# Performance work log

Hardware: AMD Instinct MI355X
Metric: run time of the kernel (lower is better)

Reference implementation:

```python
import jax, jax.numpy as jnp
import numpy as np

EMBED_DIM = 2048
NUM_HEADS = 32
NUM_KV_HEADS = 8
HEAD_DIM = EMBED_DIM // NUM_HEADS  # 64
KV_DIM = HEAD_DIM * NUM_KV_HEADS   # 512
ROPE_BASE = 10000.0


def rope_cos_sin(seq_len, dim):
    inv_freq = 1.0 / (ROPE_BASE ** (jnp.arange(0, dim, 2, dtype=jnp.float32) / dim))
    t = jnp.arange(seq_len, dtype=jnp.float32)
    freqs = jnp.outer(t, inv_freq)                 # [T, dim/2]
    emb = jnp.concatenate([freqs, freqs], axis=-1)  # [T, dim]
    return jnp.cos(emb), jnp.sin(emb)


def rotate_half(x):
    half = x.shape[-1] // 2
    return jnp.concatenate([-x[..., half:], x[..., :half]], axis=-1)


def setup_inputs() -> dict:
    key = jax.random.key(0)
    k_x, k_q, k_k, k_v, k_o = jax.random.split(key, 5)
    B, T, C = 2, 2048, EMBED_DIM
    s = 1.0 / np.sqrt(C)
    x = jax.random.normal(k_x, (B, T, C), dtype=jnp.float32)
    # Linear weights stored as [in, out]; no bias (bias=False)
    Wq = jax.random.normal(k_q, (C, EMBED_DIM), dtype=jnp.float32) * s
    Wk = jax.random.normal(k_k, (C, KV_DIM), dtype=jnp.float32) * s
    Wv = jax.random.normal(k_v, (C, KV_DIM), dtype=jnp.float32) * s
    Wo = jax.random.normal(k_o, (C, EMBED_DIM), dtype=jnp.float32) * s
    return {"x": x, "Wq": Wq, "Wk": Wk, "Wv": Wv, "Wo": Wo}


def reference(x, Wq, Wk, Wv, Wo):
    B, T, C = x.shape
    H, KVH, D = NUM_HEADS, NUM_KV_HEADS, HEAD_DIM
    scale = D ** -0.5
    rep = H // KVH

    q = (x @ Wq).reshape(B, T, H, D).transpose(0, 2, 1, 3)    # [B,H,T,D]
    k = (x @ Wk).reshape(B, T, KVH, D).transpose(0, 2, 1, 3)  # [B,KVH,T,D]
    v = (x @ Wv).reshape(B, T, KVH, D).transpose(0, 2, 1, 3)
    # repeat_interleave over head dim to expand KV heads
    k = jnp.repeat(k, rep, axis=1)  # [B,H,T,D]
    v = jnp.repeat(v, rep, axis=1)

    cos, sin = rope_cos_sin(T, D)
    cos = cos[None, None, :, :]
    sin = sin[None, None, :, :]
    q = q * cos + rotate_half(q) * sin
    k = k * cos + rotate_half(k) * sin

    att = jnp.einsum('bhtd,bhsd->bhts', q, k) * scale  # [B,H,T,T]
    att = jax.nn.softmax(att, axis=-1)                 # mask=None, dropout eval
    y = jnp.einsum('bhts,bhsd->bhtd', att, v)          # [B,H,T,D]
    y = y.transpose(0, 2, 1, 3).reshape(B, T, C)
    return y @ Wo
```

## Files before the change

kernel.cpp:

```cpp
#include <hip/hip_runtime.h>
#include <stdint.h>

#define Tn   2048
#define Cn   2048
#define Hn   32
#define KVHn 8
#define Dn   64
#define MR   4096
#define NQKV 3072
#define KD   2048

typedef __attribute__((ext_vector_type(4))) float fx4;
typedef __attribute__((ext_vector_type(8))) short frag8;

#define MFMA(a,b,c) __builtin_amdgcn_mfma_f32_16x16x32_bf16((a),(b),(c),0,0,0)

struct __align__(16) U16x8 { unsigned short s[8]; };

__device__ __forceinline__ unsigned short f2bf(float x){
  union { float f; unsigned u; } v; v.f = x;
  return (unsigned short)((v.u + 0x7FFFu + ((v.u >> 16) & 1u)) >> 16);
}
__device__ __forceinline__ float bf2f(unsigned short h){
  union { unsigned u; float f; } v; v.u = ((unsigned)h) << 16; return v.f;
}
__device__ __forceinline__ float sexp2(float x){
#if __has_builtin(__builtin_amdgcn_exp2f)
  return __builtin_amdgcn_exp2f(x);
#else
  return exp2f(x);
#endif
}
__device__ __forceinline__ unsigned cvtpk(float a, float b){
  unsigned r; asm("v_cvt_pk_bf16_f32 %0, %1, %2" : "=v"(r) : "v"(a), "v"(b)); return r;
}

typedef const __attribute__((address_space(1))) void cas1_void;
typedef __attribute__((address_space(3))) void as3_void;
__device__ __forceinline__ void gld16(const void* g, void* l){
  __builtin_amdgcn_global_load_lds((cas1_void*)g, (as3_void*)l, 16, 0, 0);
}

__global__ __launch_bounds__(256) void k_cvt(const float* __restrict__ in,
                                             unsigned short* __restrict__ out){
  size_t i = (size_t)blockIdx.x * 256 + threadIdx.x;
  float4 v = *(const float4*)(in + i * 4);
  ushort4 o; o.x = f2bf(v.x); o.y = f2bf(v.y); o.z = f2bf(v.z); o.w = f2bf(v.w);
  *(ushort4*)(out + i * 4) = o;
}

__global__ __launch_bounds__(256) void k_transW(const float* __restrict__ W0,
                                                const float* __restrict__ W1,
                                                const float* __restrict__ W2,
                                                unsigned short* __restrict__ out){
  __shared__ float tile[64][65];
  int n0 = blockIdx.x * 64, k0 = blockIdx.y * 64;
  const float* src; int col0, ld;
  if (n0 < 2048)      { src = W0; col0 = n0;        ld = 2048; }
  else if (n0 < 2560) { src = W1; col0 = n0 - 2048; ld = 512;  }
  else                { src = W2; col0 = n0 - 2560; ld = 512;  }
  int t = threadIdx.x;
  int r = t >> 2, cc = (t & 3) << 4;
  const float* p = src + (size_t)(k0 + r) * ld + col0 + cc;
  #pragma unroll
  for (int j = 0; j < 16; j += 4) {
    float4 v = *(const float4*)(p + j);
    tile[r][cc + j + 0] = v.x; tile[r][cc + j + 1] = v.y;
    tile[r][cc + j + 2] = v.z; tile[r][cc + j + 3] = v.w;
  }
  __syncthreads();
  int n = t >> 2, kc = (t & 3) << 4;
  unsigned short* q = out + (size_t)(n0 + n) * 2048 + k0 + kc;
  U16x8 o0, o1;
  #pragma unroll
  for (int j = 0; j < 8; ++j) o0.s[j] = f2bf(tile[kc + j][n]);
  #pragma unroll
  for (int j = 0; j < 8; ++j) o1.s[j] = f2bf(tile[kc + 8 + j][n]);
  *(U16x8*)(q) = o0;
  *(U16x8*)(q + 8) = o1;
}

__global__ __launch_bounds__(256) void k_ropetab(float* __restrict__ ct, float* __restrict__ st){
  int i = blockIdx.x * 256 + threadIdx.x;
  int tp = i >> 5, d = i & 31;
  float inv = powf(10000.0f, -(float)d * (1.0f/32.0f));
  float fr = (float)tp * inv;
  ct[i] = cosf(fr); st[i] = sinf(fr);
}

template<int OUT_BF16>
__global__ __launch_bounds__(256) void k_gemm(const unsigned short* __restrict__ A,
                                              const unsigned short* __restrict__ Bt,
                                              void* __restrict__ Cp,
                                              int M, int N, int K){
  __shared__ unsigned short As[128 * 64];
  __shared__ unsigned short Bs[128 * 64];
  int tid = threadIdx.x;
  int m0 = blockIdx.y * 128, n0 = blockIdx.x * 128;
  int w = tid >> 6, ln = tid & 63, lr = ln & 15, lg = ln >> 4;
  int wm = (w >> 1) * 64, wn = (w & 1) * 64;
  fx4 acc[4][4];
  #pragma unroll
  for (int i = 0; i < 4; ++i)
    #pragma unroll
    for (int j = 0; j < 4; ++j) acc[i][j] = (fx4){0.f,0.f,0.f,0.f};
  int steps = K >> 6;
  for (int kt = 0; kt < steps; ++kt) {
    int kb = kt << 6;
    #pragma unroll
    for (int it = 0; it < 4; ++it) {
      int nch = it * 256 + tid;
      int r = nch >> 3, c = (nch & 7) ^ (r & 7);
      gld16(A  + (size_t)(m0 + r) * K + kb + c * 8, (char*)As + nch * 16);
      gld16(Bt + (size_t)(n0 + r) * K + kb + c * 8, (char*)Bs + nch * 16);
    }
    __syncthreads();
    frag8 aF[4][2], bF[4][2];
    #pragma unroll
    for (int i = 0; i < 4; ++i) {
      int ra = wm + i * 16 + lr;
      int rb = wn + i * 16 + lr;
      #pragma unroll
      for (int kk = 0; kk < 2; ++kk) {
        aF[i][kk] = *(const frag8*)((const char*)As + ra * 128 + (((lg + 4*kk) ^ (ra & 7)) << 4));
        bF[i][kk] = *(const frag8*)((const char*)Bs + rb * 128 + (((lg + 4*kk) ^ (rb & 7)) << 4));
      }
    }
    #pragma unroll
    for (int kk = 0; kk < 2; ++kk)
      #pragma unroll
      for (int i = 0; i < 4; ++i)
        #pragma unroll
        for (int j = 0; j < 4; ++j)
          acc[i][j] = MFMA(aF[i][kk], bF[j][kk], acc[i][j]);
    __syncthreads();
  }
  #pragma unroll
  for (int i = 0; i < 4; ++i) {
    int row = m0 + wm + i * 16 + lg * 4;
    #pragma unroll
    for (int j = 0; j < 4; ++j) {
      int col = n0 + wn + j * 16 + lr;
      #pragma unroll
      for (int rr = 0; rr < 4; ++rr) {
        if (OUT_BF16) ((unsigned short*)Cp)[(size_t)(row + rr) * N + col] = f2bf(acc[i][j][rr]);
        else          ((float*)Cp)[(size_t)(row + rr) * N + col] = acc[i][j][rr];
      }
    }
  }
}

__global__ __launch_bounds__(256) void k_rope(unsigned short* __restrict__ qkv,
                                              const float* __restrict__ ct,
                                              const float* __restrict__ st){
  int idx = blockIdx.x * 256 + threadIdx.x;
  int p4 = idx & 7;
  int rest = idx >> 3;
  int hh = rest % 40;
  int row = rest / 40;
  int tpos = row & (Tn - 1);
  int colbase = (hh < 32) ? (hh << 6) : (2048 + ((hh - 32) << 6));
  int d0 = p4 << 2;
  unsigned short* base = qkv + (size_t)row * NQKV + colbase + d0;
  ushort4 av = *(const ushort4*)(base);
  ushort4 bv = *(const ushort4*)(base + 32);
  float4 c4 = *(const float4*)(ct + (tpos << 5) + d0);
  float4 s4 = *(const float4*)(st + (tpos << 5) + d0);
  float sc = (hh < 32) ? 0.180336880f : 1.0f;
  float a0 = bf2f(av.x), a1 = bf2f(av.y), a2 = bf2f(av.z), a3 = bf2f(av.w);
  float b0 = bf2f(bv.x), b1 = bf2f(bv.y), b2 = bf2f(bv.z), b3 = bf2f(bv.w);
  ushort4 ra, rb;
  ra.x = f2bf((a0 * c4.x - b0 * s4.x) * sc);
  ra.y = f2bf((a1 * c4.y - b1 * s4.y) * sc);
  ra.z = f2bf((a2 * c4.z - b2 * s4.z) * sc);
  ra.w = f2bf((a3 * c4.w - b3 * s4.w) * sc);
  rb.x = f2bf((b0 * c4.x + a0 * s4.x) * sc);
  rb.y = f2bf((b1 * c4.y + a1 * s4.y) * sc);
  rb.z = f2bf((b2 * c4.z + a2 * s4.z) * sc);
  rb.w = f2bf((b3 * c4.w + a3 * s4.w) * sc);
  *(ushort4*)(base)      = ra;
  *(ushort4*)(base + 32) = rb;
}

__global__ __launch_bounds__(256) void k_vt(const unsigned short* __restrict__ qkv,
                                            unsigned short* __restrict__ vt){
  __shared__ unsigned short tl[64][66];
  int head = blockIdx.y;
  int b = head >> 3, kvh = head & 7;
  int t0 = blockIdx.x * 64;
  int t = threadIdx.x;
  int r = t >> 2, cc = (t & 3) << 4;
  const unsigned short* p = qkv + (size_t)(b * Tn + t0 + r) * NQKV + 2560 + kvh * 64 + cc;
  U16x8 v0 = *(const U16x8*)(p);
  U16x8 v1 = *(const U16x8*)(p + 8);
  #pragma unroll
  for (int j = 0; j < 8; ++j) { tl[r][cc + j] = v0.s[j]; tl[r][cc + 8 + j] = v1.s[j]; }
  __syncthreads();
  int d = t >> 2, cpair = t & 3;
  unsigned short* q = vt + ((size_t)head * 64 + d) * Tn + t0;
  #pragma unroll
  for (int ci = 0; ci < 2; ++ci) {
    int c = cpair * 2 + ci;
    U16x8 oo;
    #pragma unroll
    for (int e = 0; e < 8; ++e)
      oo.s[e] = tl[32 * (c >> 2) + 16 * (e >> 2) + 4 * (c & 3) + (e & 3)][d];
    *(U16x8*)(q + c * 8) = oo;
  }
}

__global__ __launch_bounds__(256) void k_attn(const unsigned short* __restrict__ qkv,
                                              const unsigned short* __restrict__ vt,
                                              unsigned short* __restrict__ y){
  __shared__ unsigned short Ks[2][64 * 64];
  __shared__ unsigned short Vs[2][64 * 64];
  int tid = threadIdx.x, w = tid >> 6, ln = tid & 63, lq = ln & 15, lg = ln >> 4;
  int bh = blockIdx.y, b = bh >> 5, h = bh & 31, kvh = h >> 2;
  int q0 = blockIdx.x * 128;
  frag8 qF[2][2];
  #pragma unroll
  for (int s = 0; s < 2; ++s) {
    const unsigned short* qrow = qkv + (size_t)(b * Tn + q0 + w * 32 + 16 * s + lq) * NQKV + h * 64;
    qF[s][0] = *(const frag8*)(qrow + lg * 8);
    qF[s][1] = *(const frag8*)(qrow + 32 + lg * 8);
  }
  int n0 = tid, n1 = 256 + tid;
  int r0 = n0 >> 3, c0 = (n0 & 7) ^ (r0 & 7);
  int r1 = n1 >> 3, c1 = (n1 & 7) ^ (r1 & 7);
  const unsigned short* kp0 = qkv + (size_t)b * Tn * NQKV + 2048 + kvh * 64 + (size_t)r0 * NQKV + c0 * 8;
  const unsigned short* kp1 = qkv + (size_t)b * Tn * NQKV + 2048 + kvh * 64 + (size_t)r1 * NQKV + c1 * 8;
  const unsigned short* vp0 = vt + ((size_t)(b * 8 + kvh) * 64 + r0) * Tn + c0 * 8;
  const unsigned short* vp1 = vt + ((size_t)(b * 8 + kvh) * 64 + r1) * Tn + c1 * 8;
  int koff0 = lq * 128 + (((lg)     ^ (lq & 7)) << 4);
  int koff1 = lq * 128 + (((lg + 4) ^ (lq & 7)) << 4);

#define STAGE(BUF) do {                                      \
    gld16(kp0, (char*)&Ks[BUF][0] + n0 * 16);                \
    gld16(kp1, (char*)&Ks[BUF][0] + n1 * 16);                \
    gld16(vp0, (char*)&Vs[BUF][0] + n0 * 16);                \
    gld16(vp1, (char*)&Vs[BUF][0] + n1 * 16);                \
    kp0 += 64 * NQKV; kp1 += 64 * NQKV; vp0 += 64; vp1 += 64;\
  } while (0)

#define PB(S, KK) ({ union { unsigned u[4]; frag8 f; } t_;                        \
    t_.u[0] = pu[S][2*(KK)][0]; t_.u[1] = pu[S][2*(KK)][1];                       \
    t_.u[2] = pu[S][2*(KK)+1][0]; t_.u[3] = pu[S][2*(KK)+1][1]; t_.f; })

#define COMPUTE(BUF) do {                                                         \
    const char* kb_ = (const char*)&Ks[BUF][0];                                   \
    const char* vb_ = (const char*)&Vs[BUF][0];                                   \
    frag8 kf[4][2];                                                               \
    _Pragma("unroll")                                                             \
    for (int mf = 0; mf < 4; ++mf) {                                              \
      kf[mf][0] = *(const frag8*)(kb_ + mf * 2048 + koff0);                       \
      kf[mf][1] = *(const frag8*)(kb_ + mf * 2048 + koff1);                       \
    }                                                                             \
    fx4 sf[2][4];                                                                 \
    __builtin_amdgcn_s_setprio(1);                                                \
    _Pragma("unroll")                                                             \
    for (int s = 0; s < 2; ++s)                                                   \
      _Pragma("unroll")                                                           \
      for (int mf = 0; mf < 4; ++mf) {                                            \
        sf[s][mf] = (fx4){0.f, 0.f, 0.f, 0.f};                                    \
        sf[s][mf] = MFMA(kf[mf][0], qF[s][0], sf[s][mf]);                         \
        sf[s][mf] = MFMA(kf[mf][1], qF[s][1], sf[s][mf]);                         \
      }                                                                           \
    __builtin_amdgcn_s_setprio(0);                                                \
    unsigned pu[2][4][2];                                                         \
    _Pragma("unroll")                                                             \
    for (int s = 0; s < 2; ++s) {                                                 \
      float ps = 0.f;                                                             \
      _Pragma("unroll")                                                           \
      for (int mf = 0; mf < 4; ++mf) {                                            \
        float p0 = sexp2(sf[s][mf][0]);                                           \
        float p1 = sexp2(sf[s][mf][1]);                                           \
        float p2 = sexp2(sf[s][mf][2]);                                           \
        float p3 = sexp2(sf[s][mf][3]);                                           \
        ps += (p0 + p1) + (p2 + p3);                                              \
        pu[s][mf][0] = cvtpk(p0, p1);                                             \
        pu[s][mf][1] = cvtpk(p2, p3);                                             \
      }                                                                           \
      lpart[s] += ps;                                                             \
    }                                                                             \
    frag8 vf[4][2];                                                               \
    _Pragma("unroll")                                                             \
    for (int df = 0; df < 4; ++df) {                                              \
      vf[df][0] = *(const frag8*)(vb_ + df * 2048 + koff0);                       \
      vf[df][1] = *(const frag8*)(vb_ + df * 2048 + koff1);                       \
    }                                                                             \
    __builtin_amdgcn_s_setprio(1);                                                \
    _Pragma("unroll")                                                             \
    for (int s = 0; s < 2; ++s)                                                   \
      _Pragma("unroll")                                                           \
      for (int df = 0; df < 4; ++df) {                                            \
        o[s][df] = MFMA(vf[df][0], PB(s, 0), o[s][df]);                           \
        o[s][df] = MFMA(vf[df][1], PB(s, 1), o[s][df]);                           \
      }                                                                           \
    __builtin_amdgcn_s_setprio(0);                                                \
  } while (0)

  fx4 o[2][4];
  float lpart[2] = {0.f, 0.f};
  #pragma unroll
  for (int s = 0; s < 2; ++s)
    #pragma unroll
    for (int i = 0; i < 4; ++i) o[s][i] = (fx4){0.f, 0.f, 0.f, 0.f};

  STAGE(0);
  __syncthreads();
  for (int kt = 0; kt < 32; kt += 2) {
    STAGE(1);
    COMPUTE(0);
    __syncthreads();
    if (kt + 2 < 32) STAGE(0);
    COMPUTE(1);
    __syncthreads();
  }
#undef STAGE
#undef COMPUTE
#undef PB

  #pragma unroll
  for (int s = 0; s < 2; ++s) {
    lpart[s] += __shfl_xor(lpart[s], 16);
    lpart[s] += __shfl_xor(lpart[s], 32);
    float inv = 1.0f / lpart[s];
    unsigned short* yp = y + (size_t)(b * Tn + q0 + w * 32 + 16 * s + lq) * Cn + h * 64;
    #pragma unroll
    for (int df = 0; df < 4; ++df) {
      unsigned lo = cvtpk(o[s][df][0] * inv, o[s][df][1] * inv);
      unsigned hi = cvtpk(o[s][df][2] * inv, o[s][df][3] * inv);
      *(uint2*)(yp + df * 16 + lg * 4) = make_uint2(lo, hi);
    }
  }
}

extern "C" void kernel_launch(void* const* d_in, const int* in_sizes, int n_in,
                              void* d_out, int out_size, void* d_ws, size_t ws_size,
                              hipStream_t stream){
  const float* x  = (const float*)d_in[0];
  const float* Wq = (const float*)d_in[1];
  const float* Wk = (const float*)d_in[2];
  const float* Wv = (const float*)d_in[3];
  const float* Wo = (const float*)d_in[4];
  char* ws = (char*)d_ws;
  size_t off = 0;
  unsigned short* xb    = (unsigned short*)(ws + off); off += (size_t)MR * KD * 2;
  unsigned short* wqkvt = (unsigned short*)(ws + off); off += (size_t)NQKV * KD * 2;
  unsigned short* wot   = (unsigned short*)(ws + off); off += (size_t)KD * KD * 2;
  unsigned short* qkv   = (unsigned short*)(ws + off); off += (size_t)MR * NQKV * 2;
  unsigned short* vtb   = (unsigned short*)(ws + off); off += (size_t)16 * 64 * Tn * 2;
  float* ctab = (float*)(ws + off); off += (size_t)Tn * 32 * 4;
  float* stab = (float*)(ws + off); off += (size_t)Tn * 32 * 4;
  unsigned short* yb = xb;

  k_cvt<<<8192, 256, 0, stream>>>(x, xb);
  k_transW<<<dim3(48, 32), 256, 0, stream>>>(Wq, Wk, Wv, wqkvt);
  k_transW<<<dim3(32, 32), 256, 0, stream>>>(Wo, Wo, Wo, wot);
  k_ropetab<<<256, 256, 0, stream>>>(ctab, stab);
  k_gemm<1><<<dim3(NQKV / 128, MR / 128), 256, 0, stream>>>(xb, wqkvt, qkv, MR, NQKV, KD);
  k_rope<<<5120, 256, 0, stream>>>(qkv, ctab, stab);
  k_vt<<<dim3(Tn / 64, 16), 256, 0, stream>>>(qkv, vtb);
  k_attn<<<dim3(Tn / 128, 64), 256, 0, stream>>>(qkv, vtb, yb);
  k_gemm<0><<<dim3(KD / 128, MR / 128), 256, 0, stream>>>(yb, wot, d_out, MR, KD, KD);
}
```

Baseline: 227.8 us.

## Fuse RoPE and V-transpose into QKV GEMM epilogue

```diff
diff --git a/kernel.cpp b/kernel.cpp
--- a/kernel.cpp
+++ b/kernel.cpp
@@ -80,19 +80,21 @@
   *(U16x8*)(q + 8) = o1;
 }
 
-__global__ __launch_bounds__(256) void k_ropetab(float* __restrict__ ct, float* __restrict__ st){
+__global__ __launch_bounds__(256) void k_ropetab(float2* __restrict__ cs){
   int i = blockIdx.x * 256 + threadIdx.x;
   int tp = i >> 5, d = i & 31;
   float inv = powf(10000.0f, -(float)d * (1.0f/32.0f));
   float fr = (float)tp * inv;
-  ct[i] = cosf(fr); st[i] = sinf(fr);
-}
-
-template<int OUT_BF16>
+  cs[i] = make_float2(cosf(fr), sinf(fr));
+}
+
+template<int MODE>
 __global__ __launch_bounds__(256) void k_gemm(const unsigned short* __restrict__ A,
                                               const unsigned short* __restrict__ Bt,
                                               void* __restrict__ Cp,
-                                              int M, int N, int K){
+                                              int M, int N, int K,
+                                              const float2* __restrict__ cs,
+                                              unsigned short* __restrict__ vtb){
   __shared__ unsigned short As[128 * 64];
   __shared__ unsigned short Bs[128 * 64];
   int tid = threadIdx.x;
@@ -135,77 +137,59 @@
           acc[i][j] = MFMA(aF[i][kk], bF[j][kk], acc[i][j]);
     __syncthreads();
   }
-  #pragma unroll
-  for (int i = 0; i < 4; ++i) {
-    int row = m0 + wm + i * 16 + lg * 4;
-    #pragma unroll
-    for (int j = 0; j < 4; ++j) {
-      int col = n0 + wn + j * 16 + lr;
-      #pragma unroll
-      for (int rr = 0; rr < 4; ++rr) {
-        if (OUT_BF16) ((unsigned short*)Cp)[(size_t)(row + rr) * N + col] = f2bf(acc[i][j][rr]);
-        else          ((float*)Cp)[(size_t)(row + rr) * N + col] = acc[i][j][rr];
+  if (MODE == 0) {
+    #pragma unroll
+    for (int i = 0; i < 4; ++i) {
+      int row = m0 + wm + i * 16 + lg * 4;
+      #pragma unroll
+      for (int j = 0; j < 4; ++j) {
+        int col = n0 + wn + j * 16 + lr;
+        #pragma unroll
+        for (int rr = 0; rr < 4; ++rr)
+          ((float*)Cp)[(size_t)(row + rr) * N + col] = acc[i][j][rr];
       }
     }
-  }
-}
-
-__global__ __launch_bounds__(256) void k_rope(unsigned short* __restrict__ qkv,
-                                              const float* __restrict__ ct,
-                                              const float* __restrict__ st){
-  int idx = blockIdx.x * 256 + threadIdx.x;
-  int p4 = idx & 7;
-  int rest = idx >> 3;
-  int hh = rest % 40;
-  int row = rest / 40;
-  int tpos = row & (Tn - 1);
-  int colbase = (hh < 32) ? (hh << 6) : (2048 + ((hh - 32) << 6));
-  int d0 = p4 << 2;
-  unsigned short* base = qkv + (size_t)row * NQKV + colbase + d0;
-  ushort4 av = *(const ushort4*)(base);
-  ushort4 bv = *(const ushort4*)(base + 32);
-  float4 c4 = *(const float4*)(ct + (tpos << 5) + d0);
-  float4 s4 = *(const float4*)(st + (tpos << 5) + d0);
-  float sc = (hh < 32) ? 0.180336880f : 1.0f;
-  float a0 = bf2f(av.x), a1 = bf2f(av.y), a2 = bf2f(av.z), a3 = bf2f(av.w);
-  float b0 = bf2f(bv.x), b1 = bf2f(bv.y), b2 = bf2f(bv.z), b3 = bf2f(bv.w);
-  ushort4 ra, rb;
-  ra.x = f2bf((a0 * c4.x - b0 * s4.x) * sc);
-  ra.y = f2bf((a1 * c4.y - b1 * s4.y) * sc);
-  ra.z = f2bf((a2 * c4.z - b2 * s4.z) * sc);
-  ra.w = f2bf((a3 * c4.w - b3 * s4.w) * sc);
-  rb.x = f2bf((b0 * c4.x + a0 * s4.x) * sc);
-  rb.y = f2bf((b1 * c4.y + a1 * s4.y) * sc);
-  rb.z = f2bf((b2 * c4.z + a2 * s4.z) * sc);
-  rb.w = f2bf((b3 * c4.w + a3 * s4.w) * sc);
-  *(ushort4*)(base)      = ra;
-  *(ushort4*)(base + 32) = rb;
-}
-
-__global__ __launch_bounds__(256) void k_vt(const unsigned short* __restrict__ qkv,
-                                            unsigned short* __restrict__ vt){
-  __shared__ unsigned short tl[64][66];
-  int head = blockIdx.y;
-  int b = head >> 3, kvh = head & 7;
-  int t0 = blockIdx.x * 64;
-  int t = threadIdx.x;
-  int r = t >> 2, cc = (t & 3) << 4;
-  const unsigned short* p = qkv + (size_t)(b * Tn + t0 + r) * NQKV + 2560 + kvh * 64 + cc;
-  U16x8 v0 = *(const U16x8*)(p);
-  U16x8 v1 = *(const U16x8*)(p + 8);
-  #pragma unroll
-  for (int j = 0; j < 8; ++j) { tl[r][cc + j] = v0.s[j]; tl[r][cc + 8 + j] = v1.s[j]; }
-  __syncthreads();
-  int d = t >> 2, cpair = t & 3;
-  unsigned short* q = vt + ((size_t)head * 64 + d) * Tn + t0;
-  #pragma unroll
-  for (int ci = 0; ci < 2; ++ci) {
-    int c = cpair * 2 + ci;
-    U16x8 oo;
-    #pragma unroll
-    for (int e = 0; e < 8; ++e)
-      oo.s[e] = tl[32 * (c >> 2) + 16 * (e >> 2) + 4 * (c & 3) + (e & 3)][d];
-    *(U16x8*)(q + c * 8) = oo;
+  } else {
+    int nb = n0 + wn;
+    if (nb < 2560) {
+      float sc = (n0 < 2048) ? 0.180336880f : 1.0f;
+      unsigned short* outp = (unsigned short*)Cp;
+      #pragma unroll
+      for (int i = 0; i < 4; ++i) {
+        int rowb = m0 + wm + i * 16 + lg * 4;
+        #pragma unroll
+        for (int jp = 0; jp < 2; ++jp) {
+          int dA = jp * 16 + lr;
+          #pragma unroll
+          for (int rr = 0; rr < 4; ++rr) {
+            int row = rowb + rr;
+            float2 cv = cs[((row & (Tn-1)) << 5) + dA];
+            float a = acc[i][jp][rr], b = acc[i][jp + 2][rr];
+            outp[(size_t)row * N + nb + dA]      = f2bf((a * cv.x - b * cv.y) * sc);
+            outp[(size_t)row * N + nb + dA + 32] = f2bf((b * cv.x + a * cv.y) * sc);
+          }
+        }
+      }
+    } else {
+      int kvh = (nb - 2560) >> 6;
+      #pragma unroll
+      for (int i = 0; i < 4; ++i) {
+        int rowb = m0 + wm + i * 16 + lg * 4;
+        int bb = rowb >> 11;
+        int trel = rowb & (Tn - 1);
+        int t64 = trel & 63;
+        int t0 = trel - t64;
+        int a_ = t64 >> 5, b2 = (t64 >> 4) & 1, c_ = (t64 >> 2) & 3;
+        int off = (4 * a_ + c_) * 8 + 4 * b2;
+        #pragma unroll
+        for (int j = 0; j < 4; ++j) {
+          int d = j * 16 + lr;
+          unsigned lo = cvtpk(acc[i][j][0], acc[i][j][1]);
+          unsigned hi = cvtpk(acc[i][j][2], acc[i][j][3]);
+          *(uint2*)(vtb + ((size_t)(bb * 8 + kvh) * 64 + d) * Tn + t0 + off) = make_uint2(lo, hi);
+        }
+      }
+    }
   }
 }
 
@@ -350,17 +334,14 @@
   unsigned short* wot   = (unsigned short*)(ws + off); off += (size_t)KD * KD * 2;
   unsigned short* qkv   = (unsigned short*)(ws + off); off += (size_t)MR * NQKV * 2;
   unsigned short* vtb   = (unsigned short*)(ws + off); off += (size_t)16 * 64 * Tn * 2;
-  float* ctab = (float*)(ws + off); off += (size_t)Tn * 32 * 4;
-  float* stab = (float*)(ws + off); off += (size_t)Tn * 32 * 4;
+  float2* cstab = (float2*)(ws + off); off += (size_t)Tn * 32 * 8;
   unsigned short* yb = xb;
 
   k_cvt<<<8192, 256, 0, stream>>>(x, xb);
   k_transW<<<dim3(48, 32), 256, 0, stream>>>(Wq, Wk, Wv, wqkvt);
   k_transW<<<dim3(32, 32), 256, 0, stream>>>(Wo, Wo, Wo, wot);
-  k_ropetab<<<256, 256, 0, stream>>>(ctab, stab);
-  k_gemm<1><<<dim3(NQKV / 128, MR / 128), 256, 0, stream>>>(xb, wqkvt, qkv, MR, NQKV, KD);
-  k_rope<<<5120, 256, 0, stream>>>(qkv, ctab, stab);
-  k_vt<<<dim3(Tn / 64, 16), 256, 0, stream>>>(qkv, vtb);
+  k_ropetab<<<256, 256, 0, stream>>>(cstab);
+  k_gemm<2><<<dim3(NQKV / 128, MR / 128), 256, 0, stream>>>(xb, wqkvt, qkv, MR, NQKV, KD, cstab, vtb);
   k_attn<<<dim3(Tn / 128, 64), 256, 0, stream>>>(qkv, vtb, yb);
-  k_gemm<0><<<dim3(KD / 128, MR / 128), 256, 0, stream>>>(yb, wot, d_out, MR, KD, KD);
-}
+  k_gemm<0><<<dim3(KD / 128, MR / 128), 256, 0, stream>>>(yb, wot, d_out, MR, KD, KD, nullptr, nullptr);
+}
```

Result: slower. 233.7 us (+2.6%).
